# Optimization experiments

Hardware: AMD Instinct MI355X
Metric: run time of the kernel (lower is better)

The kernel has to match this reference:

```python
import jax, jax.numpy as jnp
import numpy as np

EPS = 1e-6
ROPE_THETA = 1000000.0
SPAN_LENGTHS = [700, 300, 600, 448]
L, D, H, HK, DH, FF = 2, 2048, 16, 8, 128, 8192


def _rmsnorm(x, w):
    var = jnp.mean(jnp.square(x), axis=-1, keepdims=True)
    return x * jax.lax.rsqrt(var + EPS) * w


def _rotate_half(x):
    x1, x2 = jnp.split(x, 2, axis=-1)
    return jnp.concatenate([-x2, x1], axis=-1)


def setup_inputs() -> dict:
    key = jax.random.key(0)
    ks = jax.random.split(key, 8)
    s = 0.02  # init scale
    seg = np.repeat(np.arange(len(SPAN_LENGTHS), dtype=np.int32), SPAN_LENGTHS)
    pos = np.concatenate([np.arange(n, dtype=np.int32) for n in SPAN_LENGTHS])
    T = seg.shape[0]
    return {
        "hidden_states": jax.random.normal(ks[0], (T, D), jnp.float32),
        "ln1_w": jnp.ones((L, D), jnp.float32),
        "ln2_w": jnp.ones((L, D), jnp.float32),
        "wq": jax.random.normal(ks[1], (L, D, H * DH), jnp.float32) * s,
        "wk": jax.random.normal(ks[2], (L, D, HK * DH), jnp.float32) * s,
        "wv": jax.random.normal(ks[3], (L, D, HK * DH), jnp.float32) * s,
        "wo": jax.random.normal(ks[4], (L, H * DH, D), jnp.float32) * s,
        "qn_w": jnp.ones((L, DH), jnp.float32),
        "kn_w": jnp.ones((L, DH), jnp.float32),
        "wg": jax.random.normal(ks[5], (L, D, FF), jnp.float32) * s,
        "wu": jax.random.normal(ks[6], (L, D, FF), jnp.float32) * s,
        "wd": jax.random.normal(ks[7], (L, FF, D), jnp.float32) * s,
        "final_norm_w": jnp.ones((D,), jnp.float32),
        "segment_ids": jnp.asarray(seg),
        "position_ids": jnp.asarray(pos),
    }


def reference(hidden_states, ln1_w, ln2_w, wq, wk, wv, wo, qn_w, kn_w, wg, wu, wd, final_norm_w, segment_ids, position_ids):
    T = hidden_states.shape[0]
    # rotary tables from per-request positions (positions reset per span)
    inv_freq = 1.0 / (ROPE_THETA ** (jnp.arange(0, DH, 2, dtype=jnp.float32) / DH))
    freqs = position_ids.astype(jnp.float32)[:, None] * inv_freq  # [T, DH/2]
    emb = jnp.concatenate([freqs, freqs], axis=-1)                # [T, DH]
    cos = jnp.cos(emb)[:, None, :]
    sin = jnp.sin(emb)[:, None, :]
    # ragged causal mask: attend only within the same request span, causally
    tok = jnp.arange(T)
    mask = (segment_ids[:, None] == segment_ids[None, :]) & (tok[:, None] >= tok[None, :])
    neg = jnp.finfo(hidden_states.dtype).min
    scale = 1.0 / np.sqrt(DH)

    x = hidden_states
    for l in range(L):
        h = _rmsnorm(x, ln1_w[l])
        q = (h @ wq[l]).reshape(T, H, DH)
        k = (h @ wk[l]).reshape(T, HK, DH)
        v = (h @ wv[l]).reshape(T, HK, DH)
        q = _rmsnorm(q, qn_w[l])  # Qwen3 per-head q/k RMSNorm
        k = _rmsnorm(k, kn_w[l])
        q = q * cos + _rotate_half(q) * sin
        k = k * cos + _rotate_half(k) * sin
        rep = H // HK  # GQA
        k = jnp.repeat(k, rep, axis=1)
        v = jnp.repeat(v, rep, axis=1)
        scores = jnp.einsum('thd,shd->hts', q, k) * scale  # [H, T, T]
        scores = jnp.where(mask[None], scores, neg)
        attn = jax.nn.softmax(scores, axis=-1)
        o = jnp.einsum('hts,shd->thd', attn, v).reshape(T, H * DH)
        x = x + o @ wo[l]
        h = _rmsnorm(x, ln2_w[l])
        x = x + (jax.nn.silu(h @ wg[l]) * (h @ wu[l])) @ wd[l]
    return _rmsnorm(x, final_norm_w)
```

## Files before the change

kernel.cpp:

```cpp
#include <hip/hip_runtime.h>
#include <stdint.h>

#define T_SEQ 2048
#define DMODEL 2048
#define NH 16
#define NKV 8
#define DHEAD 128
#define DFF 8192

typedef float f32x4 __attribute__((ext_vector_type(4)));
typedef float f32x2 __attribute__((ext_vector_type(2)));
typedef __bf16 bf16x8 __attribute__((ext_vector_type(8)));
typedef unsigned short ushort_t;

typedef __attribute__((address_space(1))) void gvoid;
typedef __attribute__((address_space(3))) void lvoid;

__device__ inline unsigned short f2bf(float f) {
  unsigned int u = __float_as_uint(f);
  u += 0x7fffu + ((u >> 16) & 1u);
  return (unsigned short)(u >> 16);
}
__device__ inline float bf2f(unsigned short h) {
  return __uint_as_float(((unsigned int)h) << 16);
}

__device__ inline void gload_lds16(const void* g, void* l) {
  __builtin_amdgcn_global_load_lds((gvoid*)g, (lvoid*)l, 16, 0, 0);
}

template <typename TIN>
__global__ __launch_bounds__(256) void k_transpose_bf16(const TIN* __restrict__ in,
                                                        ushort_t* __restrict__ out,
                                                        int R, int C, int rmode) {
  __shared__ float tile[64 * 72];
  int tid = threadIdx.x;
  int r0 = blockIdx.y * 64, c0 = blockIdx.x * 64;
  int rl = tid >> 4;
  int cc = tid & 15;
#pragma unroll
  for (int i = 0; i < 4; ++i) {
    int row = rl + i * 16;
    const TIN* src = in + (size_t)(r0 + row) * C + c0 + cc * 4;
    float v0, v1, v2, v3;
    if constexpr (sizeof(TIN) == 4) {
      f32x4 v = *(const f32x4*)src;
      v0 = v.x; v1 = v.y; v2 = v.z; v3 = v.w;
    } else {
      ushort4 v = *(const ushort4*)src;
      v0 = bf2f(v.x); v1 = bf2f(v.y); v2 = bf2f(v.z); v3 = bf2f(v.w);
    }
    int chunk = cc ^ (row & 15);
    f32x4 t = {v0, v1, v2, v3};
    *(f32x4*)&tile[row * 72 + chunk * 4] = t;
  }
  __syncthreads();
#pragma unroll
  for (int i = 0; i < 4; ++i) {
    int nrow = rl + i * 16;
    int k4 = cc * 4;
    ushort4 o;
    {
      int k = k4 + 0;
      o.x = f2bf(tile[k * 72 + (((nrow >> 2) ^ (k & 15)) << 2) + (nrow & 3)]);
      k = k4 + 1;
      o.y = f2bf(tile[k * 72 + (((nrow >> 2) ^ (k & 15)) << 2) + (nrow & 3)]);
      k = k4 + 2;
      o.z = f2bf(tile[k * 72 + (((nrow >> 2) ^ (k & 15)) << 2) + (nrow & 3)]);
      k = k4 + 3;
      o.w = f2bf(tile[k * 72 + (((nrow >> 2) ^ (k & 15)) << 2) + (nrow & 3)]);
    }
    int n = c0 + nrow;
    int orow = n;
    if (rmode == 1) orow = ((n >> 4) << 5) + (n & 15);
    else if (rmode == 2) orow = ((n >> 4) << 5) + 16 + (n & 15);
    *(ushort4*)(out + (size_t)orow * R + r0 + k4) = o;
  }
}

template <int BF16OUT>
__global__ __launch_bounds__(256) void k_rmsnorm(const float* __restrict__ X,
                                                 const float* __restrict__ W,
                                                 void* __restrict__ OUT) {
  int row = blockIdx.x, tid = threadIdx.x;
  const float* xr = X + (size_t)row * DMODEL;
  f32x4 x0 = *(const f32x4*)(xr + tid * 4);
  f32x4 x1 = *(const f32x4*)(xr + 1024 + tid * 4);
  float ss = x0.x * x0.x + x0.y * x0.y + x0.z * x0.z + x0.w * x0.w +
             x1.x * x1.x + x1.y * x1.y + x1.z * x1.z + x1.w * x1.w;
#pragma unroll
  for (int o = 1; o < 64; o <<= 1) ss += __shfl_xor(ss, o, 64);
  __shared__ float red[4];
  int w = tid >> 6;
  if ((tid & 63) == 0) red[w] = ss;
  __syncthreads();
  float tot = red[0] + red[1] + red[2] + red[3];
  float sc = rsqrtf(tot / (float)DMODEL + 1e-6f);
  f32x4 w0 = *(const f32x4*)(W + tid * 4);
  f32x4 w1 = *(const f32x4*)(W + 1024 + tid * 4);
  if constexpr (BF16OUT) {
    ushort_t* o = (ushort_t*)OUT + (size_t)row * DMODEL;
    ushort4 a, b;
    a.x = f2bf(x0.x * sc * w0.x); a.y = f2bf(x0.y * sc * w0.y);
    a.z = f2bf(x0.z * sc * w0.z); a.w = f2bf(x0.w * sc * w0.w);
    b.x = f2bf(x1.x * sc * w1.x); b.y = f2bf(x1.y * sc * w1.y);
    b.z = f2bf(x1.z * sc * w1.z); b.w = f2bf(x1.w * sc * w1.w);
    *(ushort4*)(o + tid * 4) = a;
    *(ushort4*)(o + 1024 + tid * 4) = b;
  } else {
    float* o = (float*)OUT + (size_t)row * DMODEL;
    f32x4 a = {x0.x * sc * w0.x, x0.y * sc * w0.y, x0.z * sc * w0.z, x0.w * sc * w0.w};
    f32x4 b = {x1.x * sc * w1.x, x1.y * sc * w1.y, x1.z * sc * w1.z, x1.w * sc * w1.w};
    *(f32x4*)(o + tid * 4) = a;
    *(f32x4*)(o + 1024 + tid * 4) = b;
  }
}

template <int NZ, int WRITEH>
__global__ __launch_bounds__(512) void k_redln(const ushort_t* __restrict__ P,
                                               const float* __restrict__ RES,
                                               const float* __restrict__ W,
                                               float* __restrict__ OUT,
                                               ushort_t* __restrict__ HB) {
  int row = blockIdx.x, tid = threadIdx.x;
  size_t base = (size_t)row * DMODEL + tid * 4;
  f32x4 v = *(const f32x4*)(RES + base);
#pragma unroll
  for (int z = 0; z < NZ; ++z) {
    ushort4 t = *(const ushort4*)(P + (size_t)z * T_SEQ * DMODEL + base);
    v.x += bf2f(t.x); v.y += bf2f(t.y); v.z += bf2f(t.z); v.w += bf2f(t.w);
  }
  *(f32x4*)(OUT + base) = v;
  if constexpr (WRITEH) {
    float ss = v.x * v.x + v.y * v.y + v.z * v.z + v.w * v.w;
#pragma unroll
    for (int o = 1; o < 64; o <<= 1) ss += __shfl_xor(ss, o, 64);
    __shared__ float red[8];
    if ((tid & 63) == 0) red[tid >> 6] = ss;
    __syncthreads();
    float tot = 0.f;
#pragma unroll
    for (int i = 0; i < 8; ++i) tot += red[i];
    float sc = rsqrtf(tot / (float)DMODEL + 1e-6f);
    f32x4 wv = *(const f32x4*)(W + tid * 4);
    ushort4 h;
    h.x = f2bf(v.x * sc * wv.x); h.y = f2bf(v.y * sc * wv.y);
    h.z = f2bf(v.z * sc * wv.z); h.w = f2bf(v.w * sc * wv.w);
    *(ushort4*)(HB + base) = h;
  }
}

#define EPI_STOREB 3
#define EPI_GLU 5

#define LOAD_B256(bs, rbase)                                                   \
  {                                                                            \
    _Pragma("unroll") for (int ks = 0; ks < 2; ++ks)                           \
        _Pragma("unroll") for (int ni = 0; ni < 2; ++ni)                       \
            bfr[ks][ni] = *(const bf16x8*)((bs) +                              \
                (((rbase) + ni * 16 + lr) << 6) +                              \
                ((((ks << 2) + lg) ^ (lr & 7)) << 3));                         \
  }

#define MFMA_Q256(q)                                                           \
  {                                                                            \
    _Pragma("unroll") for (int ks = 0; ks < 2; ++ks)                           \
        _Pragma("unroll") for (int mi = 0; mi < 4; ++mi)                       \
            _Pragma("unroll") for (int ni = 0; ni < 2; ++ni)                   \
                acc[mi][(q) * 2 + ni] =                                        \
                    __builtin_amdgcn_mfma_f32_16x16x32_bf16(                   \
                        af[ks][mi], bfr[ks][ni], acc[mi][(q) * 2 + ni], 0, 0, 0); \
  }

template <int LAST>
__device__ __forceinline__ void g256_iter(
    const ushort_t* __restrict__ as, const ushort_t* __restrict__ bsA,
    const ushort_t* __restrict__ bsB, ushort_t* __restrict__ nA,
    ushort_t* __restrict__ nB, const ushort_t* __restrict__ an,
    const ushort_t* __restrict__ bn, size_t rs, int slds, int lr, int lg,
    f32x4 (&acc)[4][8]) {
  bf16x8 af[2][4], bfr[2][2];
#pragma unroll
  for (int ks = 0; ks < 2; ++ks)
#pragma unroll
    for (int mi = 0; mi < 4; ++mi)
      af[ks][mi] = *(const bf16x8*)(as + ((mi * 16 + lr) << 6) +
                                    ((((ks << 2) + lg) ^ (lr & 7)) << 3));
  LOAD_B256(bsA, 0);
  if constexpr (!LAST) {
    gload_lds16(an, nA + slds);
    gload_lds16(an + rs, nA + 4096 + slds);
    gload_lds16(bn, nB + slds);
    gload_lds16(bn + 2 * rs, nB + 8192 + slds);
  }
  __builtin_amdgcn_s_barrier();
  asm volatile("s_waitcnt lgkmcnt(0)" ::: "memory");
  __builtin_amdgcn_sched_barrier(0);
  __builtin_amdgcn_s_setprio(1);
  MFMA_Q256(0);
  __builtin_amdgcn_s_setprio(0);
  LOAD_B256(bsA, 32);
  if constexpr (!LAST) {
    gload_lds16(an + 2 * rs, nA + 8192 + slds);
    gload_lds16(an + 3 * rs, nA + 12288 + slds);
    gload_lds16(bn + rs, nB + 4096 + slds);
    gload_lds16(bn + 3 * rs, nB + 12288 + slds);
    asm volatile("s_waitcnt vmcnt(8)" ::: "memory");
  } else {
    asm volatile("s_waitcnt vmcnt(0)" ::: "memory");
  }
  __builtin_amdgcn_s_barrier();
  asm volatile("s_waitcnt lgkmcnt(0)" ::: "memory");
  __builtin_amdgcn_sched_barrier(0);
  __builtin_amdgcn_s_setprio(1);
  MFMA_Q256(1);
  __builtin_amdgcn_s_setprio(0);
  LOAD_B256(bsB, 0);
  __builtin_amdgcn_s_barrier();
  asm volatile("s_waitcnt lgkmcnt(0)" ::: "memory");
  __builtin_amdgcn_sched_barrier(0);
  __builtin_amdgcn_s_setprio(1);
  MFMA_Q256(2);
  __builtin_amdgcn_s_setprio(0);
  LOAD_B256(bsB, 32);
  if constexpr (!LAST) {
    asm volatile("s_waitcnt vmcnt(2)" ::: "memory");
  }
  __builtin_amdgcn_s_barrier();
  asm volatile("s_waitcnt lgkmcnt(0)" ::: "memory");
  __builtin_amdgcn_sched_barrier(0);
  __builtin_amdgcn_s_setprio(1);
  MFMA_Q256(3);
  __builtin_amdgcn_s_setprio(0);
  __builtin_amdgcn_s_barrier();
}

template <int EPI>
__global__ __launch_bounds__(512, 2) void k_gemm256(
    const ushort_t* __restrict__ A, const ushort_t* __restrict__ BT,
    ushort_t* __restrict__ CB, int N, int Kstride, int Kc, size_t zoff) {
  __shared__ ushort_t lds[65536];
  const int tid = threadIdx.x;
  const int l = tid & 63, wid = tid >> 6;
  const int wm = wid >> 1, wn = wid & 1;
  const int lr = l & 15, lg = l >> 4;
  const int gx = gridDim.x;
  const int nwg = gx * gridDim.y;
  const int bid = blockIdx.x + gx * blockIdx.y;
  const int chunk = nwg >> 3;
  const int x = bid & 7;
  const int local = bid >> 3;
  const int cn = chunk >> 2;
  const int ncx = gx / cn;
  const int m0 = ((x / ncx) * 4 + local / cn) * 256;
  const int n0 = ((x % ncx) * cn + local % cn) * 256;
  const int z = blockIdx.z;
  const int NT = Kc >> 6;

  A += (size_t)z * Kc;
  BT += (size_t)z * Kc;
  CB += (size_t)z * zoff;

  const int srow = tid >> 3;
  const int scs = (tid & 7) ^ (srow & 7);
  const size_t sgoff = (size_t)srow * Kstride + scs * 8;
  const int slds = wid * 512;

  const ushort_t* ga = A + (size_t)m0 * Kstride + sgoff;
  const ushort_t* gb = BT + (size_t)n0 * Kstride + sgoff;
  const size_t rs = (size_t)64 * Kstride;

  f32x4 acc[4][8] = {};

  ushort_t* Ab0 = lds;
  ushort_t* Bb0 = lds + 16384;
  ushort_t* Ab1 = lds + 32768;
  ushort_t* Bb1 = lds + 49152;

  gload_lds16(ga, Ab0 + slds);
  gload_lds16(ga + rs, Ab0 + 4096 + slds);
  gload_lds16(gb, Bb0 + slds);
  gload_lds16(gb + 2 * rs, Bb0 + 8192 + slds);
  gload_lds16(ga + 2 * rs, Ab0 + 8192 + slds);
  gload_lds16(ga + 3 * rs, Ab0 + 12288 + slds);
  gload_lds16(gb + rs, Bb0 + 4096 + slds);
  gload_lds16(gb + 3 * rs, Bb0 + 12288 + slds);
  asm volatile("s_waitcnt vmcnt(2)" ::: "memory");
  __builtin_amdgcn_s_barrier();

  for (int kt = 0; kt < NT - 1; ++kt) {
    const int d = kt & 1;
    const ushort_t* as = (d ? Ab1 : Ab0) + wm * 4096;
    const ushort_t* bsA = (d ? Bb1 : Bb0) + (wn * 2) * 4096;
    ushort_t* nA = d ? Ab0 : Ab1;
    ushort_t* nB = d ? Bb0 : Bb1;
    g256_iter<0>(as, bsA, bsA + 4096, nA, nB, ga + (size_t)(kt + 1) * 64,
                 gb + (size_t)(kt + 1) * 64, rs, slds, lr, lg, acc);
  }
  {
    const int d = (NT - 1) & 1;
    const ushort_t* as = (d ? Ab1 : Ab0) + wm * 4096;
    const ushort_t* bsA = (d ? Bb1 : Bb0) + (wn * 2) * 4096;
    g256_iter<1>(as, bsA, bsA + 4096, nullptr, nullptr, nullptr, nullptr, rs,
                 slds, lr, lg, acc);
  }

  if constexpr (EPI == EPI_GLU) {
#pragma unroll
    for (int mi = 0; mi < 4; ++mi)
#pragma unroll
      for (int ci = 0; ci < 8; ci += 2)
#pragma unroll
        for (int rr = 0; rr < 4; ++rr) {
          int m = m0 + wm * 64 + mi * 16 + lg * 4 + rr;
          int nblk = n0 + wn * 128 + ci * 16;
          int col = ((nblk >> 5) << 4) + lr;
          float gv = acc[mi][ci][rr];
          float uv = acc[mi][ci + 1][rr];
          float s = gv / (1.f + __expf(-gv));
          CB[(size_t)m * 8192 + col] = f2bf(s * uv);
        }
  } else {
#pragma unroll
    for (int mi = 0; mi < 4; ++mi)
#pragma unroll
      for (int ci = 0; ci < 8; ++ci)
#pragma unroll
        for (int rr = 0; rr < 4; ++rr) {
          int m = m0 + wm * 64 + mi * 16 + lg * 4 + rr;
          int n = n0 + wn * 128 + ci * 16 + lr;
          CB[(size_t)m * N + n] = f2bf(acc[mi][ci][rr]);
        }
  }
}

__global__ __launch_bounds__(256) void k_qkv_post(const ushort_t* __restrict__ Q0,
                                                  const ushort_t* __restrict__ Q1,
                                                  const float* __restrict__ QNW,
                                                  const float* __restrict__ KNW,
                                                  const int* __restrict__ POS,
                                                  ushort_t* __restrict__ Qb,
                                                  ushort_t* __restrict__ Kb,
                                                  ushort_t* __restrict__ Vb) {
  int t = blockIdx.x;
  int tid = threadIdx.x;
  int w = tid >> 6, l = tid & 63;
  float pos = (float)POS[t];
  const ushort_t* base0 = Q0 + (size_t)t * 4096;
  const ushort_t* base1 = Q1 + (size_t)t * 4096;
  int i0 = 2 * (l & 31);
  const float K2 = 19.931568569324174f / 64.f;
  float ang0 = pos * exp2f(-(float)i0 * K2);
  float ang1 = pos * exp2f(-(float)(i0 + 1) * K2);
  float cs0 = cosf(ang0), sn0 = sinf(ang0);
  float cs1 = cosf(ang1), sn1 = sinf(ang1);
#pragma unroll
  for (int si = 0; si < 8; ++si) {
    int slot = w + si * 4;
    ushort2 xa = *(const ushort2*)(base0 + slot * 128 + l * 2);
    ushort2 xb = *(const ushort2*)(base1 + slot * 128 + l * 2);
    float v0 = bf2f(xa.x) + bf2f(xb.x), v1 = bf2f(xa.y) + bf2f(xb.y);
    float ss = v0 * v0 + v1 * v1;
#pragma unroll
    for (int o = 1; o < 64; o <<= 1) ss += __shfl_xor(ss, o, 64);
    if (slot < 24) {
      float sc = rsqrtf(ss / 128.f + 1e-6f);
      const float* wn = (slot < 16) ? QNW : KNW;
      f32x2 wv = *(const f32x2*)(wn + l * 2);
      v0 = v0 * sc * wv.x;
      v1 = v1 * sc * wv.y;
      float p0 = __shfl_xor(v0, 32, 64);
      float p1 = __shfl_xor(v1, 32, 64);
      float r0 = (l < 32) ? -p0 : p0;
      float r1 = (l < 32) ? -p1 : p1;
      v0 = v0 * cs0 + r0 * sn0;
      v1 = v1 * cs1 + r1 * sn1;
    }
    ushort2 uv;
    uv.x = f2bf(v0);
    uv.y = f2bf(v1);
    ushort_t* dst;
    if (slot < 16)
      dst = Qb + (size_t)t * 2048 + slot * 128 + l * 2;
    else if (slot < 24)
      dst = Kb + (size_t)t * 1024 + (slot - 16) * 128 + l * 2;
    else
      dst = Vb + (size_t)t * 1024 + (slot - 24) * 128 + l * 2;
    *(ushort2*)dst = uv;
  }
}

__global__ __launch_bounds__(64) void k_flash(const ushort_t* __restrict__ Qb,
                                              const ushort_t* __restrict__ Kb,
                                              const ushort_t* __restrict__ VT,
                                              const int* __restrict__ SEG,
                                              ushort_t* __restrict__ Ob) {
  __shared__ ushort_t Pl[2][16 * 40];
  int l = threadIdx.x;
  int qt = blockIdx.x, kvh = blockIdx.y;
  int q0 = qt * 16;
  int lr = l & 15, lg = l >> 4;
  int h0 = kvh * 2;
  bf16x8 qf0[4], qf1[4];
  {
    const bf16x8* qv = (const bf16x8*)(Qb + (size_t)(q0 + lr) * 2048 + h0 * 128);
#pragma unroll
    for (int kk = 0; kk < 4; ++kk) {
      qf0[kk] = qv[kk * 4 + lg];
      qf1[kk] = qv[16 + kk * 4 + lg];
    }
  }
  int segq[4];
#pragma unroll
  for (int r = 0; r < 4; ++r) segq[r] = SEG[q0 + lg * 4 + r];
  int target = SEG[q0];
  int lo = 0, hi = q0;
  while (lo < hi) {
    int mid = (lo + hi) >> 1;
    if (SEG[mid] < target) lo = mid + 1; else hi = mid;
  }
  int s_start = lo & ~31;
  float mr[2][4], lrun[2][4];
  f32x4 acc[2][8] = {};
#pragma unroll
  for (int h = 0; h < 2; ++h)
#pragma unroll
    for (int r = 0; r < 4; ++r) { mr[h][r] = -1e30f; lrun[h][r] = 0.f; }
  const float scale = 0.08838834764831845f;
  for (int s0 = s_start; s0 < q0 + 16; s0 += 32) {
    int sa = s0 + lr, sb = s0 + 16 + lr;
    int sac = min(sa, T_SEQ - 1), sbc = min(sb, T_SEQ - 1);
    bf16x8 vfr[8];
    int sbase = min(s0 + lg * 8, T_SEQ - 8);
#pragma unroll
    for (int c = 0; c < 8; ++c)
      vfr[c] = *(const bf16x8*)(VT + (size_t)(kvh * 128 + c * 16 + lr) * T_SEQ + sbase);
    f32x4 SA0 = {}, SB0 = {}, SA1 = {}, SB1 = {};
    const bf16x8* ka = (const bf16x8*)(Kb + (size_t)sac * 1024 + kvh * 128);
    const bf16x8* kb_ = (const bf16x8*)(Kb + (size_t)sbc * 1024 + kvh * 128);
#pragma unroll
    for (int kk = 0; kk < 4; ++kk) {
      bf16x8 kaf = ka[kk * 4 + lg];
      bf16x8 kbf = kb_[kk * 4 + lg];
      SA0 = __builtin_amdgcn_mfma_f32_16x16x32_bf16(qf0[kk], kaf, SA0, 0, 0, 0);
      SB0 = __builtin_amdgcn_mfma_f32_16x16x32_bf16(qf0[kk], kbf, SB0, 0, 0, 0);
      SA1 = __builtin_amdgcn_mfma_f32_16x16x32_bf16(qf1[kk], kaf, SA1, 0, 0, 0);
      SB1 = __builtin_amdgcn_mfma_f32_16x16x32_bf16(qf1[kk], kbf, SB1, 0, 0, 0);
    }
    int sga = SEG[sac], sgb = SEG[sbc];
    bool mAv[4], mBv[4];
#pragma unroll
    for (int r = 0; r < 4; ++r) {
      int qrow = q0 + lg * 4 + r;
      mAv[r] = (sa <= qrow) && (sga == segq[r]);
      mBv[r] = (sb <= qrow) && (sgb == segq[r]);
    }
#pragma unroll
    for (int h = 0; h < 2; ++h) {
#pragma unroll
      for (int r = 0; r < 4; ++r) {
        float sva = (h ? SA1[r] : SA0[r]);
        float svb = (h ? SB1[r] : SB0[r]);
        float xa = mAv[r] ? sva * scale : -1e30f;
        float xb = mBv[r] ? svb * scale : -1e30f;
        float mx = fmaxf(xa, xb);
#pragma unroll
        for (int o = 1; o < 16; o <<= 1) mx = fmaxf(mx, __shfl_xor(mx, o, 64));
        float nm = fmaxf(mr[h][r], mx);
        float ea = __expf(xa - nm), eb = __expf(xb - nm);
        float rsum = ea + eb;
#pragma unroll
        for (int o = 1; o < 16; o <<= 1) rsum += __shfl_xor(rsum, o, 64);
        float al = __expf(mr[h][r] - nm);
        lrun[h][r] = lrun[h][r] * al + rsum;
        mr[h][r] = nm;
#pragma unroll
        for (int c = 0; c < 8; ++c) acc[h][c][r] *= al;
        Pl[h][(lg * 4 + r) * 40 + lr] = f2bf(ea);
        Pl[h][(lg * 4 + r) * 40 + 16 + lr] = f2bf(eb);
      }
    }
    asm volatile("s_waitcnt lgkmcnt(0)" ::: "memory");
    bf16x8 pa0 = *(const bf16x8*)&Pl[0][lr * 40 + lg * 8];
    bf16x8 pa1 = *(const bf16x8*)&Pl[1][lr * 40 + lg * 8];
#pragma unroll
    for (int c = 0; c < 8; ++c) {
      acc[0][c] = __builtin_amdgcn_mfma_f32_16x16x32_bf16(pa0, vfr[c], acc[0][c], 0, 0, 0);
      acc[1][c] = __builtin_amdgcn_mfma_f32_16x16x32_bf16(pa1, vfr[c], acc[1][c], 0, 0, 0);
    }
  }
#pragma unroll
  for (int h = 0; h < 2; ++h)
#pragma unroll
    for (int c = 0; c < 8; ++c)
#pragma unroll
      for (int r = 0; r < 4; ++r) {
        float ov = acc[h][c][r] / lrun[h][r];
        Ob[(size_t)(q0 + lg * 4 + r) * 2048 + (h0 + h) * 128 + c * 16 + lr] = f2bf(ov);
      }
}

extern "C" void kernel_launch(void* const* d_in, const int* in_sizes, int n_in,
                              void* d_out, int out_size, void* d_ws, size_t ws_size,
                              hipStream_t stream) {
  const float* hidden = (const float*)d_in[0];
  const float* ln1 = (const float*)d_in[1];
  const float* ln2 = (const float*)d_in[2];
  const float* wq = (const float*)d_in[3];
  const float* wk = (const float*)d_in[4];
  const float* wv = (const float*)d_in[5];
  const float* wo = (const float*)d_in[6];
  const float* qnw = (const float*)d_in[7];
  const float* knw = (const float*)d_in[8];
  const float* wg = (const float*)d_in[9];
  const float* wu = (const float*)d_in[10];
  const float* wd = (const float*)d_in[11];
  const float* fnw = (const float*)d_in[12];
  const int* seg = (const int*)d_in[13];
  const int* pos = (const int*)d_in[14];
  float* out = (float*)d_out;

  char* ws = (char*)d_ws;
  size_t off = 0;
  auto alloc = [&](size_t bytes) {
    char* p = ws + off;
    off += (bytes + 255) & ~(size_t)255;
    return p;
  };
  ushort_t* wT = (ushort_t*)alloc((size_t)2 * DFF * DMODEL * 2);
  ushort_t* hbuf = (ushort_t*)alloc((size_t)T_SEQ * DMODEL * 2);
  ushort_t* qb = (ushort_t*)alloc((size_t)T_SEQ * 2048 * 2);
  ushort_t* kb = (ushort_t*)alloc((size_t)T_SEQ * 1024 * 2);
  ushort_t* vb = (ushort_t*)alloc((size_t)T_SEQ * 1024 * 2);
  ushort_t* vT = (ushort_t*)alloc((size_t)T_SEQ * 1024 * 2);
  ushort_t* ob = (ushort_t*)alloc((size_t)T_SEQ * 2048 * 2);
  ushort_t* qkvp = (ushort_t*)alloc((size_t)2 * T_SEQ * 4096 * 2);
  ushort_t* pbuf = (ushort_t*)alloc((size_t)4 * T_SEQ * DMODEL * 2);
  ushort_t* mbuf = (ushort_t*)alloc((size_t)T_SEQ * DFF * 2);
  (void)ws_size; (void)in_sizes; (void)n_in; (void)out_size;

  dim3 b256(256), b64(64), b512(512);
  k_rmsnorm<1><<<T_SEQ, b256, 0, stream>>>(hidden, ln1, hbuf);

  for (int lyr = 0; lyr < 2; ++lyr) {
    const float* xsrc = (lyr == 0) ? hidden : out;

    const float* wql = wq + (size_t)lyr * DMODEL * 2048;
    const float* wkl = wk + (size_t)lyr * DMODEL * 1024;
    const float* wvl = wv + (size_t)lyr * DMODEL * 1024;
    k_transpose_bf16<float><<<dim3(32, 32), b256, 0, stream>>>(wql, wT, 2048, 2048, 0);
    k_transpose_bf16<float><<<dim3(16, 32), b256, 0, stream>>>(wkl, wT + (size_t)2048 * 2048, 2048, 1024, 0);
    k_transpose_bf16<float><<<dim3(16, 32), b256, 0, stream>>>(wvl, wT + (size_t)3072 * 2048, 2048, 1024, 0);
    k_gemm256<EPI_STOREB><<<dim3(16, 8, 2), b512, 0, stream>>>(
        hbuf, wT, qkvp, 4096, 2048, 1024, (size_t)2048 * 4096);
    k_qkv_post<<<T_SEQ, b256, 0, stream>>>(qkvp, qkvp + (size_t)2048 * 4096,
                                           qnw + (size_t)lyr * 128, knw + (size_t)lyr * 128,
                                           pos, qb, kb, vb);
    k_transpose_bf16<ushort_t><<<dim3(16, 32), b256, 0, stream>>>(vb, vT, 2048, 1024, 0);
    k_flash<<<dim3(T_SEQ / 16, NKV), b64, 0, stream>>>(qb, kb, vT, seg, ob);

    const float* wol = wo + (size_t)lyr * 2048 * DMODEL;
    k_transpose_bf16<float><<<dim3(32, 32), b256, 0, stream>>>(wol, wT, 2048, 2048, 0);
    k_gemm256<EPI_STOREB><<<dim3(8, 8, 4), b512, 0, stream>>>(
        ob, wT, pbuf, 2048, 2048, 512, (size_t)2048 * 2048);
    k_redln<4, 1><<<T_SEQ, b512, 0, stream>>>(pbuf, xsrc,
                                              ln2 + (size_t)lyr * DMODEL, out, hbuf);

    const float* wgl = wg + (size_t)lyr * DMODEL * DFF;
    const float* wul = wu + (size_t)lyr * DMODEL * DFF;
    const float* wdl = wd + (size_t)lyr * DFF * DMODEL;
    k_transpose_bf16<float><<<dim3(128, 32), b256, 0, stream>>>(wgl, wT, 2048, 8192, 1);
    k_transpose_bf16<float><<<dim3(128, 32), b256, 0, stream>>>(wul, wT, 2048, 8192, 2);
    k_gemm256<EPI_GLU><<<dim3(64, 8, 1), b512, 0, stream>>>(
        hbuf, wT, mbuf, 16384, 2048, 2048, 0);
    k_transpose_bf16<float><<<dim3(32, 128), b256, 0, stream>>>(wdl, wT, 8192, 2048, 0);
    k_gemm256<EPI_STOREB><<<dim3(8, 8, 4), b512, 0, stream>>>(
        mbuf, wT, pbuf, 2048, 8192, 2048, (size_t)2048 * 2048);
    if (lyr == 0) {
      k_redln<4, 1><<<T_SEQ, b512, 0, stream>>>(pbuf, out, ln1 + DMODEL, out, hbuf);
    } else {
      k_redln<4, 0><<<T_SEQ, b512, 0, stream>>>(pbuf, out, nullptr, out, nullptr);
    }
  }
  k_rmsnorm<0><<<T_SEQ, b256, 0, stream>>>(out, fnw, out);
}
```

Measured before the change: 830.9 us.

## Double-buffer B fragments and drop intra-iteration barriers in 256 GEMM loop

Restructures the GEMM main-loop iteration so B register fragments are double-buffered (b0/b1), letting the next LDS read be issued before the current MFMA quarter runs. All eight global-to-LDS prefetches are issued up front, and the four per-quarter workgroup barriers are replaced by partial lgkmcnt waits, leaving a single vmcnt(0) wait and barrier at the end of each iteration. The aim is to cut synchronization stalls and overlap LDS reads with MFMA work. The costs are more VGPR pressure and waiting for all global loads to finish at the end of each iteration instead of draining them gradually, which could expose memory latency.

```diff
diff --git a/kernel.cpp b/kernel.cpp
--- a/kernel.cpp
+++ b/kernel.cpp
@@ -153,23 +153,23 @@
 #define EPI_STOREB 3
 #define EPI_GLU 5
 
-#define LOAD_B256(bs, rbase)                                                   \
+#define LOADB(dst, bs, rbase)                                                  \
   {                                                                            \
     _Pragma("unroll") for (int ks = 0; ks < 2; ++ks)                           \
         _Pragma("unroll") for (int ni = 0; ni < 2; ++ni)                       \
-            bfr[ks][ni] = *(const bf16x8*)((bs) +                              \
+            dst[ks][ni] = *(const bf16x8*)((bs) +                              \
                 (((rbase) + ni * 16 + lr) << 6) +                              \
                 ((((ks << 2) + lg) ^ (lr & 7)) << 3));                         \
   }
 
-#define MFMA_Q256(q)                                                           \
+#define MFMA_Q(q, B)                                                           \
   {                                                                            \
     _Pragma("unroll") for (int ks = 0; ks < 2; ++ks)                           \
         _Pragma("unroll") for (int mi = 0; mi < 4; ++mi)                       \
             _Pragma("unroll") for (int ni = 0; ni < 2; ++ni)                   \
                 acc[mi][(q) * 2 + ni] =                                        \
                     __builtin_amdgcn_mfma_f32_16x16x32_bf16(                   \
-                        af[ks][mi], bfr[ks][ni], acc[mi][(q) * 2 + ni], 0, 0, 0); \
+                        af[ks][mi], B[ks][ni], acc[mi][(q) * 2 + ni], 0, 0, 0); \
   }
 
 template <int LAST>
@@ -179,60 +179,51 @@
     ushort_t* __restrict__ nB, const ushort_t* __restrict__ an,
     const ushort_t* __restrict__ bn, size_t rs, int slds, int lr, int lg,
     f32x4 (&acc)[4][8]) {
-  bf16x8 af[2][4], bfr[2][2];
+  bf16x8 af[2][4], b0[2][2], b1[2][2];
 #pragma unroll
   for (int ks = 0; ks < 2; ++ks)
 #pragma unroll
     for (int mi = 0; mi < 4; ++mi)
       af[ks][mi] = *(const bf16x8*)(as + ((mi * 16 + lr) << 6) +
                                     ((((ks << 2) + lg) ^ (lr & 7)) << 3));
-  LOAD_B256(bsA, 0);
+  LOADB(b0, bsA, 0);
   if constexpr (!LAST) {
     gload_lds16(an, nA + slds);
     gload_lds16(an + rs, nA + 4096 + slds);
+    gload_lds16(an + 2 * rs, nA + 8192 + slds);
+    gload_lds16(an + 3 * rs, nA + 12288 + slds);
     gload_lds16(bn, nB + slds);
+    gload_lds16(bn + rs, nB + 4096 + slds);
     gload_lds16(bn + 2 * rs, nB + 8192 + slds);
-  }
-  __builtin_amdgcn_s_barrier();
+    gload_lds16(bn + 3 * rs, nB + 12288 + slds);
+  }
+  LOADB(b1, bsA, 32);
+  asm volatile("s_waitcnt lgkmcnt(4)" ::: "memory");
+  __builtin_amdgcn_sched_barrier(0);
+  __builtin_amdgcn_s_setprio(1);
+  MFMA_Q(0, b0);
+  __builtin_amdgcn_s_setprio(0);
+  LOADB(b0, bsB, 0);
+  asm volatile("s_waitcnt lgkmcnt(4)" ::: "memory");
+  __builtin_amdgcn_sched_barrier(0);
+  __builtin_amdgcn_s_setprio(1);
+  MFMA_Q(1, b1);
+  __builtin_amdgcn_s_setprio(0);
+  LOADB(b1, bsB, 32);
+  asm volatile("s_waitcnt lgkmcnt(4)" ::: "memory");
+  __builtin_amdgcn_sched_barrier(0);
+  __builtin_amdgcn_s_setprio(1);
+  MFMA_Q(2, b0);
+  __builtin_amdgcn_s_setprio(0);
   asm volatile("s_waitcnt lgkmcnt(0)" ::: "memory");
   __builtin_amdgcn_sched_barrier(0);
   __builtin_amdgcn_s_setprio(1);
-  MFMA_Q256(0);
+  MFMA_Q(3, b1);
   __builtin_amdgcn_s_setprio(0);
-  LOAD_B256(bsA, 32);
   if constexpr (!LAST) {
-    gload_lds16(an + 2 * rs, nA + 8192 + slds);
-    gload_lds16(an + 3 * rs, nA + 12288 + slds);
-    gload_lds16(bn + rs, nB + 4096 + slds);
-    gload_lds16(bn + 3 * rs, nB + 12288 + slds);
-    asm volatile("s_waitcnt vmcnt(8)" ::: "memory");
-  } else {
     asm volatile("s_waitcnt vmcnt(0)" ::: "memory");
-  }
-  __builtin_amdgcn_s_barrier();
-  asm volatile("s_waitcnt lgkmcnt(0)" ::: "memory");
-  __builtin_amdgcn_sched_barrier(0);
-  __builtin_amdgcn_s_setprio(1);
-  MFMA_Q256(1);
-  __builtin_amdgcn_s_setprio(0);
-  LOAD_B256(bsB, 0);
-  __builtin_amdgcn_s_barrier();
-  asm volatile("s_waitcnt lgkmcnt(0)" ::: "memory");
-  __builtin_amdgcn_sched_barrier(0);
-  __builtin_amdgcn_s_setprio(1);
-  MFMA_Q256(2);
-  __builtin_amdgcn_s_setprio(0);
-  LOAD_B256(bsB, 32);
-  if constexpr (!LAST) {
-    asm volatile("s_waitcnt vmcnt(2)" ::: "memory");
-  }
-  __builtin_amdgcn_s_barrier();
-  asm volatile("s_waitcnt lgkmcnt(0)" ::: "memory");
-  __builtin_amdgcn_sched_barrier(0);
-  __builtin_amdgcn_s_setprio(1);
-  MFMA_Q256(3);
-  __builtin_amdgcn_s_setprio(0);
-  __builtin_amdgcn_s_barrier();
+    __builtin_amdgcn_s_barrier();
+  }
 }
 
 template <int EPI>
@@ -279,13 +270,13 @@
 
   gload_lds16(ga, Ab0 + slds);
   gload_lds16(ga + rs, Ab0 + 4096 + slds);
-  gload_lds16(gb, Bb0 + slds);
-  gload_lds16(gb + 2 * rs, Bb0 + 8192 + slds);
   gload_lds16(ga + 2 * rs, Ab0 + 8192 + slds);
   gload_lds16(ga + 3 * rs, Ab0 + 12288 + slds);
+  gload_lds16(gb, Bb0 + slds);
   gload_lds16(gb + rs, Bb0 + 4096 + slds);
+  gload_lds16(gb + 2 * rs, Bb0 + 8192 + slds);
   gload_lds16(gb + 3 * rs, Bb0 + 12288 + slds);
-  asm volatile("s_waitcnt vmcnt(2)" ::: "memory");
+  asm volatile("s_waitcnt vmcnt(0)" ::: "memory");
   __builtin_amdgcn_s_barrier();
 
   for (int kt = 0; kt < NT - 1; ++kt) {
```

Measured after the change: 826.8 us. No clear change (-0.5%).
